# Kernel optimization log

Hardware: AMD Instinct MI355X
Metric: run time of the kernel (lower is better)

Reference implementation:

```python
import jax, jax.numpy as jnp
import numpy as np

BN_EPS = 1e-5


def _batchnorm(x, gamma, beta):
    # BatchNorm1d in training mode: stats over the flattened (b*n) batch axis, biased variance
    mean = jnp.mean(x, axis=0)
    var = jnp.var(x, axis=0)
    return gamma * (x - mean) * jax.lax.rsqrt(var + BN_EPS) + beta


def setup_inputs() -> dict:
    key = jax.random.key(0)
    ks = jax.random.split(key, 8)
    b, n, d = 4, 4096, 256
    h = d // 2
    s1 = 1.0 / np.sqrt(3.0)
    s2 = 1.0 / np.sqrt(h)
    s3 = 1.0 / np.sqrt(d)
    return {
        "xyz": jax.random.normal(ks[0], (b, n, 3), dtype=jnp.float32),
        "features": jax.random.normal(ks[1], (b, n, d), dtype=jnp.float32),
        # point_net: Linear(3,h) -> BN(h) -> ReLU -> Linear(h,d) -> BN(d) -> ReLU
        "W1": jax.random.normal(ks[2], (3, h), dtype=jnp.float32) * s1,
        "b1": jnp.zeros((h,), dtype=jnp.float32),
        "g1": jnp.ones((h,), dtype=jnp.float32),
        "be1": jnp.zeros((h,), dtype=jnp.float32),
        "W2": jax.random.normal(ks[3], (h, d), dtype=jnp.float32) * s2,
        "b2": jnp.zeros((d,), dtype=jnp.float32),
        "g2": jnp.ones((d,), dtype=jnp.float32),
        "be2": jnp.zeros((d,), dtype=jnp.float32),
        # attention projections, no bias; stored as (in, out) so x @ W == torch Linear
        "Wq": jax.random.normal(ks[4], (d, d), dtype=jnp.float32) * s3,
        "Wk": jax.random.normal(ks[5], (d, d), dtype=jnp.float32) * s3,
        "Wv": jax.random.normal(ks[6], (d, d), dtype=jnp.float32) * s3,
    }


def reference(xyz, features, W1, b1, g1, be1, W2, b2, g2, be2, Wq, Wk, Wv):
    b, n, _ = xyz.shape
    x = xyz.reshape(b * n, 3)
    h1 = jax.nn.relu(_batchnorm(x @ W1 + b1, g1, be1))       # [b*n, d/2]
    pos_enc = jax.nn.relu(_batchnorm(h1 @ W2 + b2, g2, be2)) # [b*n, d]
    f = pos_enc.reshape(b, n, -1) + features                 # [b, n, d]
    q = f @ Wq
    k = f @ Wk
    v = f @ Wv
    scale = 1.0 / np.sqrt(q.shape[-1]).astype(np.float32)
    weights = jax.nn.softmax(jnp.einsum('bnd,bmd->bnm', q, k) * scale, axis=-1)
    return jnp.einsum('bnm,bmd->bnd', weights, v)
```

## Files before the change

kernel.cpp:

```cpp
#include <hip/hip_runtime.h>
#include <hip/hip_bf16.h>
#include <math.h>

#define NROWS 16384
#define DDIM  256
#define HDIM  128
#define NSEQ  4096
#define NB    4

typedef unsigned short u16;
typedef __attribute__((ext_vector_type(8)))  short short8;
typedef __attribute__((ext_vector_type(16))) float f32x16;

#define OFF_MOM   0
#define OFF_S1    16
#define OFF_T1    144
#define OFF_CSUM  272
#define OFF_CSQ   528
#define OFF_S2    784
#define OFF_T2    1040
#define OFF_H2F   2048
#define OFF_Q     (OFF_H2F + NROWS*DDIM)
#define OFF_K     (OFF_Q  + NROWS*DDIM/2)
#define OFF_VT    (OFF_K  + NROWS*DDIM/2)
#define OFF_FB    (OFF_VT + NROWS*DDIM/2)
#define OFF_WT    (OFF_FB + NROWS*DDIM/2)

__global__ void k_xyz_stats(const float* __restrict__ xyz, float* __restrict__ mom) {
  int i = blockIdx.x * blockDim.x + threadIdx.x;
  float x = xyz[3*i+0], y = xyz[3*i+1], z = xyz[3*i+2];
  float v[9] = {x, y, z, x*x, x*y, x*z, y*y, y*z, z*z};
#pragma unroll
  for (int j = 0; j < 9; ++j) {
    float s = v[j];
#pragma unroll
    for (int off = 32; off > 0; off >>= 1) s += __shfl_down(s, off);
    if ((threadIdx.x & 63) == 0) atomicAdd(&mom[j], s);
  }
}

__global__ void k_bn1_coeff(const float* __restrict__ mom, const float* __restrict__ W1,
                            const float* __restrict__ g1, const float* __restrict__ be1,
                            float* __restrict__ s1, float* __restrict__ t1) {
  int j = threadIdx.x;
  const float invN = 1.0f / NROWS;
  float mu0 = mom[0]*invN, mu1 = mom[1]*invN, mu2 = mom[2]*invN;
  float c00 = mom[3]*invN - mu0*mu0, c01 = mom[4]*invN - mu0*mu1, c02 = mom[5]*invN - mu0*mu2;
  float c11 = mom[6]*invN - mu1*mu1, c12 = mom[7]*invN - mu1*mu2, c22 = mom[8]*invN - mu2*mu2;
  float w0 = W1[j], w1 = W1[HDIM + j], w2 = W1[2*HDIM + j];
  float meanw = mu0*w0 + mu1*w1 + mu2*w2;
  float var = c00*w0*w0 + c11*w1*w1 + c22*w2*w2
            + 2.0f*(c01*w0*w1 + c02*w0*w2 + c12*w1*w2);
  float s = g1[j] * rsqrtf(var + 1e-5f);
  s1[j] = s;
  t1[j] = be1[j] - meanw * s;
}

__global__ void k_pn1(const float* __restrict__ xyz, const float* __restrict__ W1,
                      const float* __restrict__ s1, const float* __restrict__ t1,
                      float* __restrict__ h1) {
  int t = blockIdx.x * blockDim.x + threadIdx.x;
  int j = t & (HDIM-1), row = t >> 7;
  float x = xyz[3*row+0], y = xyz[3*row+1], z = xyz[3*row+2];
  float acc = x*W1[j] + y*W1[HDIM + j] + z*W1[2*HDIM + j];
  float v = fmaf(acc, s1[j], t1[j]);
  h1[t] = fmaxf(v, 0.0f);
}

template<int OM>
__global__ __launch_bounds__(256) void k_gemm(const float* __restrict__ A,
    const float* __restrict__ B, const float* __restrict__ bias,
    void* __restrict__ Cv, int M, int N, int K) {
  __shared__ float As[16][132];
  __shared__ float Bs[16][132];
  const int tid = threadIdx.x;
  const int tx = tid & 15, ty = tid >> 4;
  const int m0 = blockIdx.x * 128, n0 = blockIdx.y * 128;
  float acc[2][4][2][4] = {};

  for (int kb = 0; kb < K; kb += 16) {
    __syncthreads();
#pragma unroll
    for (int u = 0; u < 2; ++u) {
      int idx4 = tid + u * 256;
      int am = idx4 >> 2, ak = (idx4 & 3) << 2;
      float4 av = *(const float4*)&A[(size_t)(m0 + am) * K + kb + ak];
      As[ak+0][am] = av.x; As[ak+1][am] = av.y; As[ak+2][am] = av.z; As[ak+3][am] = av.w;
      int bk = idx4 >> 5, bc = (idx4 & 31) << 2;
      float4 bv = *(const float4*)&B[(size_t)(kb + bk) * N + n0 + bc];
      *(float4*)&Bs[bk][bc] = bv;
    }
    __syncthreads();
#pragma unroll
    for (int kk = 0; kk < 16; ++kk) {
      float4 a0 = *(const float4*)&As[kk][4*ty];
      float4 a1 = *(const float4*)&As[kk][64 + 4*ty];
      float4 b0 = *(const float4*)&Bs[kk][4*tx];
      float4 b1 = *(const float4*)&Bs[kk][64 + 4*tx];
      float av[2][4] = {{a0.x,a0.y,a0.z,a0.w},{a1.x,a1.y,a1.z,a1.w}};
      float bv[2][4] = {{b0.x,b0.y,b0.z,b0.w},{b1.x,b1.y,b1.z,b1.w}};
#pragma unroll
      for (int ri = 0; ri < 2; ++ri)
#pragma unroll
        for (int i = 0; i < 4; ++i)
#pragma unroll
          for (int rj = 0; rj < 2; ++rj)
#pragma unroll
            for (int j = 0; j < 4; ++j)
              acc[ri][i][rj][j] = fmaf(av[ri][i], bv[rj][j], acc[ri][i][rj][j]);
    }
  }

  if (OM == 0) {
    float* C = (float*)Cv;
#pragma unroll
    for (int ri = 0; ri < 2; ++ri)
#pragma unroll
      for (int i = 0; i < 4; ++i) {
        int r = m0 + ri*64 + 4*ty + i;
#pragma unroll
        for (int rj = 0; rj < 2; ++rj) {
          int c = n0 + rj*64 + 4*tx;
          float4 o;
          o.x = acc[ri][i][rj][0]; o.y = acc[ri][i][rj][1];
          o.z = acc[ri][i][rj][2]; o.w = acc[ri][i][rj][3];
          if (bias) { o.x += bias[c]; o.y += bias[c+1]; o.z += bias[c+2]; o.w += bias[c+3]; }
          *(float4*)&C[(size_t)r * N + c] = o;
        }
      }
  }
}

__global__ void k_colstats(const float* __restrict__ h2, float* __restrict__ cs,
                           float* __restrict__ cq) {
  int j = threadIdx.x;
  size_t r0 = (size_t)blockIdx.x * 64;
  float s = 0.f, q = 0.f;
  for (int r = 0; r < 64; ++r) {
    float v = h2[(r0 + r) * DDIM + j];
    s += v; q += v * v;
  }
  atomicAdd(&cs[j], s);
  atomicAdd(&cq[j], q);
}

__global__ void k_bn2_coeff(const float* __restrict__ cs, const float* __restrict__ cq,
                            const float* __restrict__ g2, const float* __restrict__ be2,
                            float* __restrict__ s2, float* __restrict__ t2) {
  int j = threadIdx.x;
  const float invN = 1.0f / NROWS;
  float mean = cs[j] * invN;
  float var = cq[j] * invN - mean * mean;
  float s = g2[j] * rsqrtf(var + 1e-5f);
  s2[j] = s;
  t2[j] = be2[j] - mean * s;
}

__global__ void k_makef(const float* __restrict__ h2f, const float* __restrict__ feats,
                        const float* __restrict__ s2, const float* __restrict__ t2,
                        u16* __restrict__ fb) {
  size_t i4 = (size_t)blockIdx.x * blockDim.x + threadIdx.x;
  int c = ((int)i4 & 63) << 2;
  float4 hh = *(const float4*)&h2f[i4*4];
  float4 ff = *(const float4*)&feats[i4*4];
  float4 s = *(const float4*)&s2[c];
  float4 t = *(const float4*)&t2[c];
  float a = fmaxf(fmaf(hh.x, s.x, t.x), 0.f) + ff.x;
  float b = fmaxf(fmaf(hh.y, s.y, t.y), 0.f) + ff.y;
  float d = fmaxf(fmaf(hh.z, s.z, t.z), 0.f) + ff.z;
  float e = fmaxf(fmaf(hh.w, s.w, t.w), 0.f) + ff.w;
  union { __hip_bfloat162 b2[2]; uint2 u; } pk;
  pk.b2[0] = __float22bfloat162_rn(make_float2(a, b));
  pk.b2[1] = __float22bfloat162_rn(make_float2(d, e));
  *(uint2*)&fb[i4*4] = pk.u;
}

__global__ void k_wt(const float* __restrict__ Wq, const float* __restrict__ Wk,
                     const float* __restrict__ Wv, u16* __restrict__ WT) {
  const float* W = (blockIdx.y == 0) ? Wq : (blockIdx.y == 1) ? Wk : Wv;
  __shared__ float t[32][33];
  int n0 = (blockIdx.x & 7) * 32, k0 = (blockIdx.x >> 3) * 32;
  int tx = threadIdx.x & 31, ty = threadIdx.x >> 5;
#pragma unroll
  for (int i = 0; i < 4; ++i)
    t[ty + i*8][tx] = W[(size_t)(k0 + ty + i*8) * DDIM + n0 + tx];
  __syncthreads();
#pragma unroll
  for (int i = 0; i < 4; ++i) {
    int n = ty + i*8;
    union { __hip_bfloat16 b; u16 u; } cv;
    cv.b = __float2bfloat16(t[tx][n]);
    WT[((size_t)blockIdx.y * DDIM + n0 + n) * DDIM + k0 + tx] = cv.u;
  }
}

__global__ __launch_bounds__(256, 2) void k_proj(const u16* __restrict__ fb,
    const u16* __restrict__ WT, u16* __restrict__ qb, u16* __restrict__ kb,
    u16* __restrict__ vtb) {
  const int tid = threadIdx.x;
  const int w = tid >> 6, l = tid & 63;
  const int c = l & 31, h = l >> 5;
  const int o = blockIdx.y;
  const int m0 = blockIdx.x * 128 + w * 32;
  const u16* WTo = WT + (size_t)o * DDIM * DDIM;

  f32x16 acc[8];
#pragma unroll
  for (int nt = 0; nt < 8; ++nt)
#pragma unroll
    for (int r = 0; r < 16; ++r) acc[nt][r] = 0.f;

  const u16* arow = fb  + (size_t)(m0 + c) * DDIM + h*8;
  const u16* brow = WTo + (size_t)c * DDIM + h*8;
  for (int s = 0; s < 16; ++s) {
    short8 af = *(const short8*)(arow + s*16);
#pragma unroll
    for (int nt = 0; nt < 8; ++nt) {
      short8 bf = *(const short8*)(brow + (size_t)nt*32*DDIM + s*16);
      acc[nt] = __builtin_amdgcn_mfma_f32_32x32x16_bf16(af, bf, acc[nt], 0, 0, 0);
    }
  }

  if (o < 2) {
    u16* C = o ? kb : qb;
#pragma unroll
    for (int nt = 0; nt < 8; ++nt)
#pragma unroll
      for (int r = 0; r < 16; ++r) {
        int row = m0 + (r & 3) + 8*(r >> 2) + 4*h;
        union { __hip_bfloat16 b; u16 u; } cv;
        cv.b = __float2bfloat16(acc[nt][r]);
        C[(size_t)row * DDIM + nt*32 + c] = cv.u;
      }
  } else {
    const int bi = m0 >> 12, tloc = m0 & (NSEQ - 1);
#pragma unroll
    for (int nt = 0; nt < 8; ++nt)
#pragma unroll
      for (int g = 0; g < 4; ++g) {
        int t0 = tloc + 8*g + 4*h;
        union { __hip_bfloat162 b2[2]; uint2 u; } pk;
        pk.b2[0] = __float22bfloat162_rn(make_float2(acc[nt][4*g+0], acc[nt][4*g+1]));
        pk.b2[1] = __float22bfloat162_rn(make_float2(acc[nt][4*g+2], acc[nt][4*g+3]));
        *(uint2*)&vtb[((size_t)(bi*DDIM + nt*32 + c)) * NSEQ + t0] = pk.u;
      }
  }
}

__global__ __launch_bounds__(256, 2) void k_attn(const u16* __restrict__ Qg,
    const u16* __restrict__ Kg, const u16* __restrict__ VTg, float* __restrict__ Og) {
  __shared__ float sm4[4][32];
  __shared__ float sl4[4][32];
  __shared__ float sinv[32];
  __shared__ __align__(16) float sob[4][32][64];

  const int tid = threadIdx.x;
  const int w = tid >> 6, l = tid & 63;
  const int c = l & 31, h = l >> 5;
  const int x = blockIdx.x & 7, grp = blockIdx.x >> 3;
  const int bi = x >> 1;
  const int qt = (x & 1) * 64 + grp;
  const int qrow = qt * 32 + c;
  const size_t qgbase = ((size_t)bi * NSEQ + qrow) * DDIM;

  short8 qf[16];
#pragma unroll
  for (int dblk = 0; dblk < 16; ++dblk)
    qf[dblk] = *(const short8*)(Qg + qgbase + dblk*16 + h*8);

  f32x16 oacc[8];
#pragma unroll
  for (int dt = 0; dt < 8; ++dt)
#pragma unroll
    for (int r = 0; r < 16; ++r) oacc[dt][r] = 0.f;
  float m = -1e30f, lsum = 0.f;

  const u16* __restrict__ Kb  = Kg  + (size_t)bi * NSEQ * DDIM;
  const u16* __restrict__ VTb = VTg + (size_t)bi * DDIM * NSEQ;

  for (int t = 0; t < 32; ++t) {
    const int kb = w * 1024 + t * 32;

    f32x16 st;
#pragma unroll
    for (int r = 0; r < 16; ++r) st[r] = 0.f;
    const u16* Krow = Kb + (size_t)(kb + c) * DDIM + h*8;
#pragma unroll
    for (int dblk = 0; dblk < 16; ++dblk) {
      short8 af = *(const short8*)(Krow + dblk*16);
      st = __builtin_amdgcn_mfma_f32_32x32x16_bf16(af, qf[dblk], st, 0, 0, 0);
    }

    float p[16];
#pragma unroll
    for (int r = 0; r < 16; ++r) p[r] = st[r] * 0.0625f;
    float tm = p[0];
#pragma unroll
    for (int r = 1; r < 16; ++r) tm = fmaxf(tm, p[r]);
    tm = fmaxf(tm, __shfl_xor(tm, 32));
    if (!__all(tm <= m + 8.0f)) {
      float mn = fmaxf(m, tm);
      float corr = __expf(m - mn);
      lsum *= corr;
#pragma unroll
      for (int dt = 0; dt < 8; ++dt)
#pragma unroll
        for (int r = 0; r < 16; ++r) oacc[dt][r] *= corr;
      m = mn;
    }
    float ps = 0.f;
#pragma unroll
    for (int r = 0; r < 16; ++r) { p[r] = __expf(p[r] - m); ps += p[r]; }
    ps += __shfl_xor(ps, 32);
    lsum += ps;

    short8 bfr[2];
#pragma unroll
    for (int sub = 0; sub < 2; ++sub) {
      union { __hip_bfloat162 b; unsigned int u; } cv;
      cv.b = __float22bfloat162_rn(make_float2(p[((2*sub+0)<<2)|0], p[((2*sub+0)<<2)|1]));
      unsigned int X = cv.u;
      cv.b = __float22bfloat162_rn(make_float2(p[((2*sub+0)<<2)|2], p[((2*sub+0)<<2)|3]));
      unsigned int X2 = cv.u;
      cv.b = __float22bfloat162_rn(make_float2(p[((2*sub+1)<<2)|0], p[((2*sub+1)<<2)|1]));
      unsigned int Y = cv.u;
      cv.b = __float22bfloat162_rn(make_float2(p[((2*sub+1)<<2)|2], p[((2*sub+1)<<2)|3]));
      unsigned int Y2 = cv.u;
      unsigned int sx  = __shfl_xor(X, 32),  sx2 = __shfl_xor(X2, 32);
      unsigned int sy  = __shfl_xor(Y, 32),  sy2 = __shfl_xor(Y2, 32);
      union { unsigned int u[4]; short8 s; } bfw;
      bfw.u[0] = h ? sy  : X;
      bfw.u[1] = h ? sy2 : X2;
      bfw.u[2] = h ? Y   : sx;
      bfw.u[3] = h ? Y2  : sx2;
      bfr[sub] = bfw.s;
    }
#pragma unroll
    for (int dt = 0; dt < 8; ++dt) {
      const u16* Vrow = VTb + (size_t)(dt*32 + c) * NSEQ + kb + h*8;
      short8 vf0 = *(const short8*)(Vrow);
      short8 vf1 = *(const short8*)(Vrow + 16);
      oacc[dt] = __builtin_amdgcn_mfma_f32_32x32x16_bf16(vf0, bfr[0], oacc[dt], 0, 0, 0);
      oacc[dt] = __builtin_amdgcn_mfma_f32_32x32x16_bf16(vf1, bfr[1], oacc[dt], 0, 0, 0);
    }
  }

  if (h == 0) { sm4[w][c] = m; sl4[w][c] = lsum; }
  __syncthreads();
  float M = fmaxf(fmaxf(sm4[0][c], sm4[1][c]), fmaxf(sm4[2][c], sm4[3][c]));
  float Ltot = 0.f, scl_w = 0.f;
#pragma unroll
  for (int i = 0; i < 4; ++i) {
    float e = __expf(sm4[i][c] - M);
    Ltot += sl4[i][c] * e;
    if (i == w) scl_w = e;
  }
  if (w == 0 && h == 0) sinv[c] = 1.0f / Ltot;
  __syncthreads();

  const int q = tid >> 3, ds0 = (tid & 7) * 8;
  const size_t orow = ((size_t)bi * NSEQ + qt*32 + q) * DDIM;
#pragma unroll
  for (int cc = 0; cc < 4; ++cc) {
#pragma unroll
    for (int dd = 0; dd < 2; ++dd) {
      const int dt = cc*2 + dd;
#pragma unroll
      for (int g = 0; g < 4; ++g) {
        int dloc = dd*32 + g*8 + h*4;
        float4 v4 = make_float4(oacc[dt][4*g+0]*scl_w, oacc[dt][4*g+1]*scl_w,
                                oacc[dt][4*g+2]*scl_w, oacc[dt][4*g+3]*scl_w);
        char* pdst = (char*)&sob[w][c][0] + ((dloc*4) ^ ((c&7)<<4));
        *(float4*)pdst = v4;
      }
    }
    __syncthreads();
    float r0=0,r1=0,r2=0,r3=0,r4=0,r5=0,r6=0,r7=0;
#pragma unroll
    for (int ww = 0; ww < 4; ++ww) {
      const char* base = (const char*)&sob[ww][q][0];
      float4 a = *(const float4*)(base + ((ds0*4)     ^ ((q&7)<<4)));
      float4 b = *(const float4*)(base + (((ds0+4)*4) ^ ((q&7)<<4)));
      r0+=a.x; r1+=a.y; r2+=a.z; r3+=a.w;
      r4+=b.x; r5+=b.y; r6+=b.z; r7+=b.w;
    }
    const float iv = sinv[q];
    float4 o0 = make_float4(r0*iv, r1*iv, r2*iv, r3*iv);
    float4 o1 = make_float4(r4*iv, r5*iv, r6*iv, r7*iv);
    *(float4*)&Og[orow + cc*64 + ds0]     = o0;
    *(float4*)&Og[orow + cc*64 + ds0 + 4] = o1;
    __syncthreads();
  }
}

extern "C" void kernel_launch(void* const* d_in, const int* in_sizes, int n_in,
                              void* d_out, int out_size, void* d_ws, size_t ws_size,
                              hipStream_t stream) {
  (void)in_sizes; (void)n_in; (void)out_size; (void)ws_size;
  const float* xyz   = (const float*)d_in[0];
  const float* feats = (const float*)d_in[1];
  const float* W1    = (const float*)d_in[2];
  const float* g1    = (const float*)d_in[4];
  const float* be1   = (const float*)d_in[5];
  const float* W2    = (const float*)d_in[6];
  const float* b2    = (const float*)d_in[7];
  const float* g2    = (const float*)d_in[8];
  const float* be2   = (const float*)d_in[9];
  const float* Wq    = (const float*)d_in[10];
  const float* Wk    = (const float*)d_in[11];
  const float* Wv    = (const float*)d_in[12];

  float* ws  = (float*)d_ws;
  float* mom = ws + OFF_MOM;
  float* s1  = ws + OFF_S1;   float* t1 = ws + OFF_T1;
  float* cs  = ws + OFF_CSUM; float* cq = ws + OFF_CSQ;
  float* s2  = ws + OFF_S2;   float* t2 = ws + OFF_T2;
  float* h2f = ws + OFF_H2F;
  u16* qb  = (u16*)(ws + OFF_Q);
  u16* kb  = (u16*)(ws + OFF_K);
  u16* vtb = (u16*)(ws + OFF_VT);
  u16* fb  = (u16*)(ws + OFF_FB);
  u16* wt  = (u16*)(ws + OFF_WT);
  float* out = (float*)d_out;
  float* h1  = out;

  hipMemsetAsync(ws, 0, 2048 * sizeof(float), stream);
  k_xyz_stats<<<64, 256, 0, stream>>>(xyz, mom);
  k_bn1_coeff<<<1, 128, 0, stream>>>(mom, W1, g1, be1, s1, t1);
  k_pn1<<<(NROWS*HDIM)/256, 256, 0, stream>>>(xyz, W1, s1, t1, h1);
  k_wt<<<dim3(64, 3), 256, 0, stream>>>(Wq, Wk, Wv, wt);
  k_gemm<0><<<dim3(NROWS/128, DDIM/128), 256, 0, stream>>>(h1, W2, b2, h2f, NROWS, DDIM, HDIM);
  k_colstats<<<256, 256, 0, stream>>>(h2f, cs, cq);
  k_bn2_coeff<<<1, 256, 0, stream>>>(cs, cq, g2, be2, s2, t2);
  k_makef<<<(NROWS*DDIM/4)/256, 256, 0, stream>>>(h2f, feats, s2, t2, fb);
  k_proj<<<dim3(NROWS/128, 3), 256, 0, stream>>>(fb, wt, qb, kb, vtb);
  k_attn<<<512, 256, 0, stream>>>(qb, kb, vtb, out);
}
```

Measured before the change: 447.7 us.

## Stage K/V tiles in LDS via async global-to-LDS loads with double buffering

```diff
diff --git a/kernel.cpp b/kernel.cpp
--- a/kernel.cpp
+++ b/kernel.cpp
@@ -247,20 +247,22 @@
   }
 }
 
-__global__ __launch_bounds__(256, 2) void k_attn(const u16* __restrict__ Qg,
+__device__ __forceinline__ void gload16(const void* g, void* l) {
+  __builtin_amdgcn_global_load_lds((__attribute__((address_space(1))) void*)(g),
+                                   (__attribute__((address_space(3))) void*)(l), 16, 0, 0);
+}
+
+__global__ __launch_bounds__(128, 1) void k_attn(const u16* __restrict__ Qg,
     const u16* __restrict__ Kg, const u16* __restrict__ VTg, float* __restrict__ Og) {
-  __shared__ float sm4[4][32];
-  __shared__ float sl4[4][32];
-  __shared__ float sinv[32];
-  __shared__ __align__(16) float sob[4][32][64];
-
+  __shared__ uint4 lds4[131072/16];
+  char* lds = (char*)lds4;
   const int tid = threadIdx.x;
   const int w = tid >> 6, l = tid & 63;
   const int c = l & 31, h = l >> 5;
   const int x = blockIdx.x & 7, grp = blockIdx.x >> 3;
   const int bi = x >> 1;
-  const int qt = (x & 1) * 64 + grp;
-  const int qrow = qt * 32 + c;
+  const int qt = (x & 1) * 32 + grp;
+  const int qrow = qt * 64 + w * 32 + c;
   const size_t qgbase = ((size_t)bi * NSEQ + qrow) * DDIM;
 
   short8 qf[16];
@@ -278,119 +280,127 @@
   const u16* __restrict__ Kb  = Kg  + (size_t)bi * NSEQ * DDIM;
   const u16* __restrict__ VTb = VTg + (size_t)bi * DDIM * NSEQ;
 
-  for (int t = 0; t < 32; ++t) {
-    const int kb = w * 1024 + t * 32;
-
-    f32x16 st;
-#pragma unroll
-    for (int r = 0; r < 16; ++r) st[r] = 0.f;
-    const u16* Krow = Kb + (size_t)(kb + c) * DDIM + h*8;
-#pragma unroll
-    for (int dblk = 0; dblk < 16; ++dblk) {
-      short8 af = *(const short8*)(Krow + dblk*16);
-      st = __builtin_amdgcn_mfma_f32_32x32x16_bf16(af, qf[dblk], st, 0, 0, 0);
-    }
-
-    float p[16];
-#pragma unroll
-    for (int r = 0; r < 16; ++r) p[r] = st[r] * 0.0625f;
-    float tm = p[0];
-#pragma unroll
-    for (int r = 1; r < 16; ++r) tm = fmaxf(tm, p[r]);
-    tm = fmaxf(tm, __shfl_xor(tm, 32));
-    if (!__all(tm <= m + 8.0f)) {
-      float mn = fmaxf(m, tm);
-      float corr = __expf(m - mn);
-      lsum *= corr;
-#pragma unroll
-      for (int dt = 0; dt < 8; ++dt)
-#pragma unroll
-        for (int r = 0; r < 16; ++r) oacc[dt][r] *= corr;
-      m = mn;
-    }
-    float ps = 0.f;
-#pragma unroll
-    for (int r = 0; r < 16; ++r) { p[r] = __expf(p[r] - m); ps += p[r]; }
-    ps += __shfl_xor(ps, 32);
-    lsum += ps;
-
-    short8 bfr[2];
-#pragma unroll
-    for (int sub = 0; sub < 2; ++sub) {
-      union { __hip_bfloat162 b; unsigned int u; } cv;
-      cv.b = __float22bfloat162_rn(make_float2(p[((2*sub+0)<<2)|0], p[((2*sub+0)<<2)|1]));
-      unsigned int X = cv.u;
-      cv.b = __float22bfloat162_rn(make_float2(p[((2*sub+0)<<2)|2], p[((2*sub+0)<<2)|3]));
-      unsigned int X2 = cv.u;
-      cv.b = __float22bfloat162_rn(make_float2(p[((2*sub+1)<<2)|0], p[((2*sub+1)<<2)|1]));
-      unsigned int Y = cv.u;
-      cv.b = __float22bfloat162_rn(make_float2(p[((2*sub+1)<<2)|2], p[((2*sub+1)<<2)|3]));
-      unsigned int Y2 = cv.u;
-      unsigned int sx  = __shfl_xor(X, 32),  sx2 = __shfl_xor(X2, 32);
-      unsigned int sy  = __shfl_xor(Y, 32),  sy2 = __shfl_xor(Y2, 32);
-      union { unsigned int u[4]; short8 s; } bfw;
-      bfw.u[0] = h ? sy  : X;
-      bfw.u[1] = h ? sy2 : X2;
-      bfw.u[2] = h ? Y   : sx;
-      bfw.u[3] = h ? Y2  : sx2;
-      bfr[sub] = bfw.s;
-    }
-#pragma unroll
-    for (int dt = 0; dt < 8; ++dt) {
-      const u16* Vrow = VTb + (size_t)(dt*32 + c) * NSEQ + kb + h*8;
-      short8 vf0 = *(const short8*)(Vrow);
-      short8 vf1 = *(const short8*)(Vrow + 16);
-      oacc[dt] = __builtin_amdgcn_mfma_f32_32x32x16_bf16(vf0, bfr[0], oacc[dt], 0, 0, 0);
-      oacc[dt] = __builtin_amdgcn_mfma_f32_32x32x16_bf16(vf1, bfr[1], oacc[dt], 0, 0, 0);
-    }
-  }
-
-  if (h == 0) { sm4[w][c] = m; sl4[w][c] = lsum; }
+  auto stage = [&](int t, int bf) {
+    char* base = lds + bf*65536;
+    const int kb = t * 64;
+#pragma unroll
+    for (int ii = 0; ii < 16; ++ii) {
+      int r = w*32 + ii*2 + (l>>5);
+      int gs = (l&31) ^ (r&31);
+      const u16* gp = Kb + (size_t)(kb + r)*DDIM + gs*8;
+      gload16(gp, base + (w*32 + ii*2)*512);
+    }
+#pragma unroll
+    for (int ii = 0; ii < 16; ++ii) {
+      int j = w*32 + ii*2 + (l>>5);
+      int gc = (l&31) ^ (j&31);
+      int d = 4*j + (gc>>3);
+      const u16* gp = VTb + (size_t)d*NSEQ + kb + (gc&7)*8;
+      gload16(gp, base + 32768 + (w*32 + ii*2)*512);
+    }
+  };
+
+  stage(0, 0);
   __syncthreads();
-  float M = fmaxf(fmaxf(sm4[0][c], sm4[1][c]), fmaxf(sm4[2][c], sm4[3][c]));
-  float Ltot = 0.f, scl_w = 0.f;
-#pragma unroll
-  for (int i = 0; i < 4; ++i) {
-    float e = __expf(sm4[i][c] - M);
-    Ltot += sl4[i][c] * e;
-    if (i == w) scl_w = e;
-  }
-  if (w == 0 && h == 0) sinv[c] = 1.0f / Ltot;
-  __syncthreads();
-
-  const int q = tid >> 3, ds0 = (tid & 7) * 8;
-  const size_t orow = ((size_t)bi * NSEQ + qt*32 + q) * DDIM;
-#pragma unroll
-  for (int cc = 0; cc < 4; ++cc) {
-#pragma unroll
-    for (int dd = 0; dd < 2; ++dd) {
-      const int dt = cc*2 + dd;
-#pragma unroll
-      for (int g = 0; g < 4; ++g) {
-        int dloc = dd*32 + g*8 + h*4;
-        float4 v4 = make_float4(oacc[dt][4*g+0]*scl_w, oacc[dt][4*g+1]*scl_w,
-                                oacc[dt][4*g+2]*scl_w, oacc[dt][4*g+3]*scl_w);
-        char* pdst = (char*)&sob[w][c][0] + ((dloc*4) ^ ((c&7)<<4));
-        *(float4*)pdst = v4;
+
+  const int cx = c << 4;
+  const int jlow = c >> 2, dsub8 = (c & 3) << 3;
+
+  const int NT = NSEQ / 64;
+  for (int t = 0; t < NT; ++t) {
+    const int cur = t & 1;
+    if (t+1 < NT) stage(t+1, cur^1);
+    const char* kbuf = lds + cur*65536;
+    const char* vbuf = kbuf + 32768;
+
+    f32x16 stE[2], stO[2];
+#pragma unroll
+    for (int kt = 0; kt < 2; ++kt)
+#pragma unroll
+      for (int r = 0; r < 16; ++r) { stE[kt][r] = 0.f; stO[kt][r] = 0.f; }
+#pragma unroll
+    for (int dblk = 0; dblk < 16; dblk += 2) {
+#pragma unroll
+      for (int kt = 0; kt < 2; ++kt) {
+        int rb = (kt*32 + c) * 512;
+        short8 afE = *(const short8*)(kbuf + rb + ((dblk*32 + h*16) ^ cx));
+        short8 afO = *(const short8*)(kbuf + rb + (((dblk+1)*32 + h*16) ^ cx));
+        stE[kt] = __builtin_amdgcn_mfma_f32_32x32x16_bf16(afE, qf[dblk],   stE[kt], 0, 0, 0);
+        stO[kt] = __builtin_amdgcn_mfma_f32_32x32x16_bf16(afO, qf[dblk+1], stO[kt], 0, 0, 0);
+      }
+    }
+
+#pragma unroll
+    for (int kt = 0; kt < 2; ++kt) {
+      float p[16];
+#pragma unroll
+      for (int r = 0; r < 16; ++r) p[r] = (stE[kt][r] + stO[kt][r]) * 0.0625f;
+      float tm = p[0];
+#pragma unroll
+      for (int r = 1; r < 16; ++r) tm = fmaxf(tm, p[r]);
+      tm = fmaxf(tm, __shfl_xor(tm, 32));
+      if (!__all(tm <= m + 8.0f)) {
+        float mn = fmaxf(m, tm);
+        float corr = __expf(m - mn);
+        lsum *= corr;
+#pragma unroll
+        for (int dt = 0; dt < 8; ++dt)
+#pragma unroll
+          for (int r = 0; r < 16; ++r) oacc[dt][r] *= corr;
+        m = mn;
+      }
+      float ps = 0.f;
+#pragma unroll
+      for (int r = 0; r < 16; ++r) { p[r] = __expf(p[r] - m); ps += p[r]; }
+      ps += __shfl_xor(ps, 32);
+      lsum += ps;
+
+      short8 bfr[2];
+#pragma unroll
+      for (int sub = 0; sub < 2; ++sub) {
+        union { __hip_bfloat162 b; unsigned int u; } cv;
+        cv.b = __float22bfloat162_rn(make_float2(p[((2*sub+0)<<2)|0], p[((2*sub+0)<<2)|1]));
+        unsigned int X = cv.u;
+        cv.b = __float22bfloat162_rn(make_float2(p[((2*sub+0)<<2)|2], p[((2*sub+0)<<2)|3]));
+        unsigned int X2 = cv.u;
+        cv.b = __float22bfloat162_rn(make_float2(p[((2*sub+1)<<2)|0], p[((2*sub+1)<<2)|1]));
+        unsigned int Y = cv.u;
+        cv.b = __float22bfloat162_rn(make_float2(p[((2*sub+1)<<2)|2], p[((2*sub+1)<<2)|3]));
+        unsigned int Y2 = cv.u;
+        unsigned int sx  = __shfl_xor(X, 32),  sx2 = __shfl_xor(X2, 32);
+        unsigned int sy  = __shfl_xor(Y, 32),  sy2 = __shfl_xor(Y2, 32);
+        union { unsigned int u[4]; short8 s; } bfw;
+        bfw.u[0] = h ? sy  : X;
+        bfw.u[1] = h ? sy2 : X2;
+        bfw.u[2] = h ? Y   : sx;
+        bfw.u[3] = h ? Y2  : sx2;
+        bfr[sub] = bfw.s;
+      }
+
+#pragma unroll
+      for (int dt = 0; dt < 8; ++dt) {
+        int row = dt*8 + jlow;
+        int xv  = ((dt & 3) * 8 + jlow);
+        int s0 = (dsub8 + (kt*2+0)*2 + h) ^ xv;
+        int s1 = (dsub8 + (kt*2+1)*2 + h) ^ xv;
+        short8 vf0 = *(const short8*)(vbuf + row*512 + s0*16);
+        short8 vf1 = *(const short8*)(vbuf + row*512 + s1*16);
+        oacc[dt] = __builtin_amdgcn_mfma_f32_32x32x16_bf16(vf0, bfr[0], oacc[dt], 0, 0, 0);
+        oacc[dt] = __builtin_amdgcn_mfma_f32_32x32x16_bf16(vf1, bfr[1], oacc[dt], 0, 0, 0);
       }
     }
     __syncthreads();
-    float r0=0,r1=0,r2=0,r3=0,r4=0,r5=0,r6=0,r7=0;
-#pragma unroll
-    for (int ww = 0; ww < 4; ++ww) {
-      const char* base = (const char*)&sob[ww][q][0];
-      float4 a = *(const float4*)(base + ((ds0*4)     ^ ((q&7)<<4)));
-      float4 b = *(const float4*)(base + (((ds0+4)*4) ^ ((q&7)<<4)));
-      r0+=a.x; r1+=a.y; r2+=a.z; r3+=a.w;
-      r4+=b.x; r5+=b.y; r6+=b.z; r7+=b.w;
-    }
-    const float iv = sinv[q];
-    float4 o0 = make_float4(r0*iv, r1*iv, r2*iv, r3*iv);
-    float4 o1 = make_float4(r4*iv, r5*iv, r6*iv, r7*iv);
-    *(float4*)&Og[orow + cc*64 + ds0]     = o0;
-    *(float4*)&Og[orow + cc*64 + ds0 + 4] = o1;
-    __syncthreads();
-  }
+  }
+
+  const float inv = 1.0f / lsum;
+#pragma unroll
+  for (int dt = 0; dt < 8; ++dt)
+#pragma unroll
+    for (int g = 0; g < 4; ++g) {
+      float4 o4 = make_float4(oacc[dt][4*g+0]*inv, oacc[dt][4*g+1]*inv,
+                              oacc[dt][4*g+2]*inv, oacc[dt][4*g+3]*inv);
+      *(float4*)&Og[qgbase + dt*32 + g*8 + h*4] = o4;
+    }
 }
 
 extern "C" void kernel_launch(void* const* d_in, const int* in_sizes, int n_in,
@@ -434,5 +444,5 @@
   k_bn2_coeff<<<1, 256, 0, stream>>>(cs, cq, g2, be2, s2, t2);
   k_makef<<<(NROWS*DDIM/4)/256, 256, 0, stream>>>(h2f, feats, s2, t2, fb);
   k_proj<<<dim3(NROWS/128, 3), 256, 0, stream>>>(fb, wt, qb, kb, vtb);
-  k_attn<<<512, 256, 0, stream>>>(qb, kb, vtb, out);
-}
+  k_attn<<<256, 128, 0, stream>>>(qb, kb, vtb, out);
+}
```

New measurement: 455.8 us. About the same (+1.8%).
